# Kernel tuning notes

Measured on AMD Instinct MI355X. Metric: run time of the kernel, lower is better.

## Reference

```python
import jax, jax.numpy as jnp
import numpy as np

N_EDGES = 800_000
N_NODES = 50_000
D_MODEL = 128
D_IN = 2 * D_MODEL  # received-edge aggregate concat node features


def setup_inputs() -> dict:
    key = jax.random.key(0)
    k_e, k_n, k_r, k_w = jax.random.split(key, 4)
    edges = jax.random.normal(k_e, (N_EDGES, D_MODEL), dtype=jnp.float32)
    nodes = jax.random.normal(k_n, (N_NODES, D_MODEL), dtype=jnp.float32)
    receivers = jax.random.randint(k_r, (N_EDGES,), 0, N_NODES, dtype=jnp.int64)
    # nn.Linear(d_in, d_model, bias=False); stored as [d_in, d_model] so y = x @ W
    W = jax.random.normal(k_w, (D_IN, D_MODEL), dtype=jnp.float32) * (1.0 / np.sqrt(D_IN))
    return {"edges": edges, "nodes": nodes, "receivers": receivers, "W": W}


def reference(edges, nodes, receivers, W):
    n_nodes = nodes.shape[0]
    # unsorted_mean_agg: scatter-add edges into receiver nodes, divide by counts
    seg_sum = jax.ops.segment_sum(edges, receivers, num_segments=n_nodes)  # [N, D]
    counts = jax.ops.segment_sum(
        jnp.ones((edges.shape[0],), dtype=edges.dtype), receivers, num_segments=n_nodes
    )
    agg = seg_sum / jnp.maximum(counts, 1.0)[:, None]  # segment mean
    collected = jnp.concatenate([agg, nodes], axis=-1)  # [N, 2*D]
    updated_nodes = collected @ W  # project; update_fn = identity
    return updated_nodes
```

## Files before the change

### kernel.cpp

```cpp
#include <hip/hip_runtime.h>
#include <hip/hip_bf16.h>

#define N_EDGES  800000
#define N_NODES  50000
#define D_MODEL  128
#define D_IN     256
#define CAP      64
#define NBLK_INIT 196

typedef __attribute__((ext_vector_type(8))) short short8;
typedef __attribute__((ext_vector_type(4))) float f32x4;

static __device__ __forceinline__ unsigned short f2bf(float f) {
    unsigned int u = __builtin_bit_cast(unsigned int, f);
    u += 0x7FFFu + ((u >> 16) & 1u);
    return (unsigned short)(u >> 16);
}

__global__ __launch_bounds__(256) void init_kernel(
    int* __restrict__ cnt, const float* __restrict__ W,
    unsigned short* __restrict__ Wt)
{
    int g = blockIdx.x * 256 + threadIdx.x;
    if (g < N_NODES) cnt[g] = 0;
    if (g < D_IN * D_MODEL) {
        int k = g >> 7;
        int c = g & 127;
        Wt[c * 256 + k] = f2bf(W[g]);
    }
}

__global__ __launch_bounds__(256) void scatter_idx_kernel(
    const int* __restrict__ recv, int* __restrict__ cnt, int* __restrict__ eidx)
{
    int stride = gridDim.x * blockDim.x;
    for (int e = blockIdx.x * blockDim.x + threadIdx.x; e < N_EDGES; e += stride) {
        int node = recv[e];
        int p = atomicAdd(&cnt[node], 1);
        if (p < CAP) eidx[(node << 6) + p] = e;
    }
}

#define LDK 264

__global__ __launch_bounds__(256) void fused_agg_gemm_kernel(
    const f32x4*          __restrict__ edges4,
    const int*            __restrict__ cnt,
    const int*            __restrict__ eidx,
    const float*          __restrict__ nodes,
    const unsigned short* __restrict__ Wt,
    float*                __restrict__ out)
{
    __shared__ unsigned short As[64][LDK];

    const int t = threadIdx.x;
    const int rowBase = blockIdx.x * 64;
    const int wv   = t >> 6;
    const int lane = t & 63;
    const int sub  = lane >> 5;
    const int col4 = lane & 31;

    int cnt_l = 0;
    if (lane < 16) {
        int nn = rowBase + wv * 16 + lane;
        if (nn < N_NODES) cnt_l = cnt[nn];
    }

    #pragma unroll
    for (int it = 0; it < 4; ++it) {
        int chunk = it * 256 + t;
        int r  = chunk >> 4;
        int c8 = (chunk & 15) * 8;
        int gr = rowBase + r;
        float4 v0 = make_float4(0.f, 0.f, 0.f, 0.f);
        float4 v1 = make_float4(0.f, 0.f, 0.f, 0.f);
        if (gr < N_NODES) {
            const float* p = nodes + (size_t)gr * 128 + c8;
            v0 = *(const float4*)p;
            v1 = *(const float4*)(p + 4);
        }
        short8 s;
        s[0] = (short)f2bf(v0.x); s[1] = (short)f2bf(v0.y);
        s[2] = (short)f2bf(v0.z); s[3] = (short)f2bf(v0.w);
        s[4] = (short)f2bf(v1.x); s[5] = (short)f2bf(v1.y);
        s[6] = (short)f2bf(v1.z); s[7] = (short)f2bf(v1.w);
        *(short8*)&As[r][128 + c8] = s;
    }

    int ei_cur = 0;
    {
        int m0 = __shfl(cnt_l, 0, 64); if (m0 > CAP) m0 = CAP;
        int nn = rowBase + wv * 16;
        if (lane < m0) ei_cur = eidx[(nn << 6) + lane];
    }

    for (int i = 0; i < 16; ++i) {
        int r    = wv * 16 + i;
        int node = rowBase + r;
        int m    = __shfl(cnt_l, i, 64);
        if (m > CAP) m = CAP;

        int ei_next = 0;
        if (i < 15) {
            int mn = __shfl(cnt_l, i + 1, 64); if (mn > CAP) mn = CAP;
            if (lane < mn) ei_next = eidx[((node + 1) << 6) + lane];
        }

        f32x4 acc = {0.f, 0.f, 0.f, 0.f};

        int e = 0;
        for (; e + 16 <= m; e += 16) {
            int   idx[8];
            f32x4 v[8];
            #pragma unroll
            for (int j = 0; j < 8; ++j)
                idx[j] = __shfl(ei_cur, e + 2 * j + sub, 64);
            #pragma unroll
            for (int j = 0; j < 8; ++j)
                v[j] = __builtin_nontemporal_load(edges4 + (size_t)idx[j] * 32 + col4);
            #pragma unroll
            for (int j = 0; j < 8; ++j) acc += v[j];
        }
        for (; e + 8 <= m; e += 8) {
            int i0 = __shfl(ei_cur, e + 0 + sub, 64);
            int i1 = __shfl(ei_cur, e + 2 + sub, 64);
            int i2 = __shfl(ei_cur, e + 4 + sub, 64);
            int i3 = __shfl(ei_cur, e + 6 + sub, 64);
            f32x4 v0 = __builtin_nontemporal_load(edges4 + (size_t)i0 * 32 + col4);
            f32x4 v1 = __builtin_nontemporal_load(edges4 + (size_t)i1 * 32 + col4);
            f32x4 v2 = __builtin_nontemporal_load(edges4 + (size_t)i2 * 32 + col4);
            f32x4 v3 = __builtin_nontemporal_load(edges4 + (size_t)i3 * 32 + col4);
            acc += v0 + v1 + v2 + v3;
        }
        for (; e + 2 <= m; e += 2) {
            int i0 = __shfl(ei_cur, e + sub, 64);
            f32x4 v = __builtin_nontemporal_load(edges4 + (size_t)i0 * 32 + col4);
            acc += v;
        }
        if (e < m) {
            int i0 = __shfl(ei_cur, e, 64);
            if (sub == 0) {
                f32x4 v = __builtin_nontemporal_load(edges4 + (size_t)i0 * 32 + col4);
                acc += v;
            }
        }

        acc.x += __shfl_xor(acc.x, 32, 64);
        acc.y += __shfl_xor(acc.y, 32, 64);
        acc.z += __shfl_xor(acc.z, 32, 64);
        acc.w += __shfl_xor(acc.w, 32, 64);

        if (sub == 0) {
            float inv = 1.0f / fmaxf((float)m, 1.0f);
            ushort4 w;
            w.x = f2bf(acc.x * inv); w.y = f2bf(acc.y * inv);
            w.z = f2bf(acc.z * inv); w.w = f2bf(acc.w * inv);
            *(ushort4*)&As[r][col4 * 4] = w;
        }
        ei_cur = ei_next;
    }
    __syncthreads();

    const int lr = lane & 15;
    const int kb = lane >> 4;

    short8 a[8];
    #pragma unroll
    for (int ks = 0; ks < 8; ++ks)
        a[ks] = *(const short8*)&As[wv * 16 + lr][ks * 32 + kb * 8];

    #pragma unroll
    for (int cp = 0; cp < 4; ++cp) {
        int ct0 = cp * 2, ct1 = cp * 2 + 1;
        short8 b0[8], b1[8];
        #pragma unroll
        for (int ks = 0; ks < 8; ++ks) {
            b0[ks] = *(const short8*)(Wt + (size_t)(ct0 * 16 + lr) * 256 + ks * 32 + kb * 8);
            b1[ks] = *(const short8*)(Wt + (size_t)(ct1 * 16 + lr) * 256 + ks * 32 + kb * 8);
        }
        f32x4 acc0 = {0.f, 0.f, 0.f, 0.f};
        f32x4 acc1 = {0.f, 0.f, 0.f, 0.f};
        #pragma unroll
        for (int ks = 0; ks < 8; ++ks) {
            acc0 = __builtin_amdgcn_mfma_f32_16x16x32_bf16(a[ks], b0[ks], acc0, 0, 0, 0);
            acc1 = __builtin_amdgcn_mfma_f32_16x16x32_bf16(a[ks], b1[ks], acc1, 0, 0, 0);
        }
        #pragma unroll
        for (int r = 0; r < 4; ++r) {
            int gr = rowBase + wv * 16 + kb * 4 + r;
            if (gr < N_NODES) {
                out[(size_t)gr * 128 + ct0 * 16 + lr] = acc0[r];
                out[(size_t)gr * 128 + ct1 * 16 + lr] = acc1[r];
            }
        }
    }
}

extern "C" void kernel_launch(void* const* d_in, const int* in_sizes, int n_in,
                              void* d_out, int out_size, void* d_ws, size_t ws_size,
                              hipStream_t stream) {
    const float* edges = (const float*)d_in[0];
    const float* nodes = (const float*)d_in[1];
    const int*   recv  = (const int*)d_in[2];
    const float* W     = (const float*)d_in[3];
    float* out = (float*)d_out;

    char* base = (char*)d_ws;
    size_t o = 0;
    auto alloc = [&](size_t bytes) {
        size_t r = o; o = (o + bytes + 255) & ~(size_t)255; return r;
    };
    int*            cnt  = (int*)(base + alloc(N_NODES * 4));
    int*            eidx = (int*)(base + alloc((size_t)N_NODES * CAP * 4));
    unsigned short* Wt   = (unsigned short*)(base + alloc(D_IN * D_MODEL * 2));

    init_kernel<<<dim3(NBLK_INIT), dim3(256), 0, stream>>>(cnt, W, Wt);
    scatter_idx_kernel<<<dim3(2048), dim3(256), 0, stream>>>(recv, cnt, eidx);
    fused_agg_gemm_kernel<<<dim3((N_NODES + 63) / 64), dim3(256), 0, stream>>>(
        (const f32x4*)edges, cnt, eidx, nodes, Wt, out);
}
```

Measured before the change: 172.1 us.

## Software-pipeline edge gathers across nodes with double-buffered register prefetch

Restructures the per-node aggregation loop into a fully unrolled, double-buffered pipeline. The first 16 edges of the next node are gathered while the current node is accumulated, and edge indices are prefetched two nodes ahead. Tail handling uses masked weights instead of separate remainder loops. This hides gather latency across node boundaries, at the cost of more registers and wasted loads for nodes with fewer than 16 edges (mask reads index 0 / lane-zero values).

```diff
diff --git a/kernel.cpp b/kernel.cpp
--- a/kernel.cpp
+++ b/kernel.cpp
@@ -59,10 +59,11 @@
     const int lane = t & 63;
     const int sub  = lane >> 5;
     const int col4 = lane & 31;
+    const int nodeBase = rowBase + wv * 16;
 
     int cnt_l = 0;
     if (lane < 16) {
-        int nn = rowBase + wv * 16 + lane;
+        int nn = nodeBase + lane;
         if (nn < N_NODES) cnt_l = cnt[nn];
     }
 
@@ -87,61 +88,52 @@
         *(short8*)&As[r][128 + c8] = s;
     }
 
-    int ei_cur = 0;
-    {
-        int m0 = __shfl(cnt_l, 0, 64); if (m0 > CAP) m0 = CAP;
-        int nn = rowBase + wv * 16;
-        if (lane < m0) ei_cur = eidx[(nn << 6) + lane];
-    }
-
-    for (int i = 0; i < 16; ++i) {
-        int r    = wv * 16 + i;
-        int node = rowBase + r;
-        int m    = __shfl(cnt_l, i, 64);
-        if (m > CAP) m = CAP;
-
-        int ei_next = 0;
-        if (i < 15) {
-            int mn = __shfl(cnt_l, i + 1, 64); if (mn > CAP) mn = CAP;
-            if (lane < mn) ei_next = eidx[((node + 1) << 6) + lane];
-        }
+    auto getm = [&](int j) -> int {
+        int m = __shfl(cnt_l, j, 64);
+        return (m > CAP) ? CAP : m;
+    };
+    auto load_ei = [&](int j) -> int {
+        int m = getm(j);
+        int v = 0;
+        if (lane < m) v = eidx[((size_t)(nodeBase + j) << 6) + lane];
+        return v;
+    };
+    auto issue8 = [&](int ei, int ebase, f32x4* v) {
+        #pragma unroll
+        for (int k = 0; k < 8; ++k) {
+            int idx = __shfl(ei, ebase + 2 * k + sub, 64);
+            v[k] = __builtin_nontemporal_load(edges4 + (size_t)idx * 32 + col4);
+        }
+    };
+    auto accum8 = [&](const f32x4* v, int ebase, int m, f32x4& acc) {
+        #pragma unroll
+        for (int k = 0; k < 8; ++k) {
+            float w = (ebase + 2 * k + sub < m) ? 1.0f : 0.0f;
+            acc += v[k] * w;
+        }
+    };
+
+    f32x4 va[8], vb[8];
+
+    auto step = [&](int i, f32x4* vcur, f32x4* vnxt, int ecur, int enxt) -> int {
+        int m = getm(i);
+        if (i < 15) issue8(enxt, 0, vnxt);
+        int eC = (i < 14) ? load_ei(i + 2) : 0;
 
         f32x4 acc = {0.f, 0.f, 0.f, 0.f};
-
-        int e = 0;
-        for (; e + 16 <= m; e += 16) {
-            int   idx[8];
-            f32x4 v[8];
+        accum8(vcur, 0, m, acc);
+
+        for (int e = 16; e < m; e += 8) {
+            f32x4 vt[4];
             #pragma unroll
-            for (int j = 0; j < 8; ++j)
-                idx[j] = __shfl(ei_cur, e + 2 * j + sub, 64);
+            for (int k = 0; k < 4; ++k) {
+                int idx = __shfl(ecur, e + 2 * k + sub, 64);
+                vt[k] = __builtin_nontemporal_load(edges4 + (size_t)idx * 32 + col4);
+            }
             #pragma unroll
-            for (int j = 0; j < 8; ++j)
-                v[j] = __builtin_nontemporal_load(edges4 + (size_t)idx[j] * 32 + col4);
-            #pragma unroll
-            for (int j = 0; j < 8; ++j) acc += v[j];
-        }
-        for (; e + 8 <= m; e += 8) {
-            int i0 = __shfl(ei_cur, e + 0 + sub, 64);
-            int i1 = __shfl(ei_cur, e + 2 + sub, 64);
-            int i2 = __shfl(ei_cur, e + 4 + sub, 64);
-            int i3 = __shfl(ei_cur, e + 6 + sub, 64);
-            f32x4 v0 = __builtin_nontemporal_load(edges4 + (size_t)i0 * 32 + col4);
-            f32x4 v1 = __builtin_nontemporal_load(edges4 + (size_t)i1 * 32 + col4);
-            f32x4 v2 = __builtin_nontemporal_load(edges4 + (size_t)i2 * 32 + col4);
-            f32x4 v3 = __builtin_nontemporal_load(edges4 + (size_t)i3 * 32 + col4);
-            acc += v0 + v1 + v2 + v3;
-        }
-        for (; e + 2 <= m; e += 2) {
-            int i0 = __shfl(ei_cur, e + sub, 64);
-            f32x4 v = __builtin_nontemporal_load(edges4 + (size_t)i0 * 32 + col4);
-            acc += v;
-        }
-        if (e < m) {
-            int i0 = __shfl(ei_cur, e, 64);
-            if (sub == 0) {
-                f32x4 v = __builtin_nontemporal_load(edges4 + (size_t)i0 * 32 + col4);
-                acc += v;
+            for (int k = 0; k < 4; ++k) {
+                float w = (e + 2 * k + sub < m) ? 1.0f : 0.0f;
+                acc += vt[k] * w;
             }
         }
 
@@ -155,10 +147,34 @@
             ushort4 w;
             w.x = f2bf(acc.x * inv); w.y = f2bf(acc.y * inv);
             w.z = f2bf(acc.z * inv); w.w = f2bf(acc.w * inv);
-            *(ushort4*)&As[r][col4 * 4] = w;
-        }
-        ei_cur = ei_next;
-    }
+            *(ushort4*)&As[wv * 16 + i][col4 * 4] = w;
+        }
+        return eC;
+    };
+
+    int e0 = load_ei(0);
+    int e1 = load_ei(1);
+    int e2;
+    issue8(e0, 0, va);
+
+    e2 = step(0,  va, vb, e0, e1);
+    e0 = step(1,  vb, va, e1, e2);
+    e1 = step(2,  va, vb, e2, e0);
+    e2 = step(3,  vb, va, e0, e1);
+    e0 = step(4,  va, vb, e1, e2);
+    e1 = step(5,  vb, va, e2, e0);
+    e2 = step(6,  va, vb, e0, e1);
+    e0 = step(7,  vb, va, e1, e2);
+    e1 = step(8,  va, vb, e2, e0);
+    e2 = step(9,  vb, va, e0, e1);
+    e0 = step(10, va, vb, e1, e2);
+    e1 = step(11, vb, va, e2, e0);
+    e2 = step(12, va, vb, e0, e1);
+    e0 = step(13, vb, va, e1, e2);
+    e1 = step(14, va, vb, e2, e0);
+    e2 = step(15, vb, va, e0, e1);
+    (void)e2;
+
     __syncthreads();
 
     const int lr = lane & 15;
```

Result: no change. 172.3 us (+0.1%).
